# Kernel tuning notes

Measured on AMD Instinct MI355X. Metric: run time of the kernel, lower is better.

## Reference

```python
import jax, jax.numpy as jnp
import numpy as np

BATCH, SEQ_LEN, D_MODEL, STATE = 4, 2048, 64, 64


def setup_inputs() -> dict:
    key = jax.random.key(0)
    ks = jax.random.split(key, 6)
    def w(k, shape):
        return (jax.random.normal(k, shape, jnp.float32) * 0.05)
    return {
        "x": jax.random.normal(ks[0], (BATCH, SEQ_LEN, D_MODEL), jnp.float32),
        "W1": w(ks[1], (D_MODEL, D_MODEL)),  # fc1: d -> d (delta)
        "b1": jnp.zeros((D_MODEL,), jnp.float32),
        "W2": w(ks[2], (D_MODEL, STATE)),    # fc2: d -> n (B)
        "b2": jnp.zeros((STATE,), jnp.float32),
        "W3": w(ks[3], (D_MODEL, STATE)),    # fc3: d -> n (C)
        "b3": jnp.zeros((STATE,), jnp.float32),
        "A": w(ks[4], (D_MODEL, STATE)),     # A parameter [d, n]
    }


def reference(x, W1, b1, W2, b2, W3, b3, A):
    # x: [b, l, d]
    Bm = x @ W2 + b2                               # [b, l, n]
    C = x @ W3 + b3                                # [b, l, n]
    delta = jax.nn.softplus(x @ W1 + b1)           # [b, l, d]
    # discretization (as in original torch code)
    dA = jnp.exp(jnp.einsum('bld,dn->bldn', delta, A))   # [b, l, d, n]
    dB = delta[..., None] * Bm[:, :, None, :]            # [b, l, d, n]
    # h_prev is zeros in the original forward, so dA * h_prev == 0
    h = dA * 0.0 + x[..., None] * dB                     # [b, l, d, n]
    y = jnp.einsum('bln,bldn->bld', C, h)                # [b, l, d]
    return y
```

## Files before the change

### kernel.cpp

```cpp
#include <hip/hip_runtime.h>
#include <cmath>

#define BATCH 4
#define SEQLEN 2048
#define DMODEL 64
#define NTOK (BATCH * SEQLEN)
#define TOK_PER_WAVE 8
#define WAVES_PER_BLOCK 4
#define TOK_PER_BLOCK (TOK_PER_WAVE * WAVES_PER_BLOCK)
#define NBLOCKS (NTOK / TOK_PER_BLOCK)
#define WROW 68

__global__ __launch_bounds__(256, 1) void s6_fused_kernel(
    const float* __restrict__ x,
    const float* __restrict__ W1, const float* __restrict__ b1,
    const float* __restrict__ W2, const float* __restrict__ b2,
    const float* __restrict__ W3, const float* __restrict__ b3,
    float* __restrict__ y)
{
    __shared__ float sWT[3][DMODEL * WROW];

    const int tid = threadIdx.x;

    {
        const float4* gm[3] = { (const float4*)W1, (const float4*)W2, (const float4*)W3 };
        #pragma unroll
        for (int m = 0; m < 3; ++m) {
            #pragma unroll
            for (int i0 = 0; i0 < 4; ++i0) {
                const int i = tid + 256 * i0;
                const float4 w = gm[m][i];
                const int k  = i >> 4;
                const int d0 = (i & 15) << 2;
                sWT[m][(d0 + 0) * WROW + k] = w.x;
                sWT[m][(d0 + 1) * WROW + k] = w.y;
                sWT[m][(d0 + 2) * WROW + k] = w.z;
                sWT[m][(d0 + 3) * WROW + k] = w.w;
            }
        }
    }

    const int lane = tid & 63;
    const int wave = tid >> 6;
    const int tok0 = __builtin_amdgcn_readfirstlane(
        (blockIdx.x * WAVES_PER_BLOCK + wave) * TOK_PER_WAVE);
    const float* __restrict__ xb = x + (size_t)tok0 * DMODEL;

    float xv[TOK_PER_WAVE];
    #pragma unroll
    for (int t = 0; t < TOK_PER_WAVE; ++t)
        xv[t] = x[(size_t)(tok0 + t) * DMODEL + lane];

    float a1[TOK_PER_WAVE], a2[TOK_PER_WAVE], a3[TOK_PER_WAVE];
    const float bb1 = b1[lane], bb2 = b2[lane], bb3 = b3[lane];
    #pragma unroll
    for (int t = 0; t < TOK_PER_WAVE; ++t) { a1[t] = bb1; a2[t] = bb2; a3[t] = bb3; }

    __syncthreads();

    const float* __restrict__ r1 = &sWT[0][lane * WROW];
    const float* __restrict__ r2 = &sWT[1][lane * WROW];
    const float* __restrict__ r3 = &sWT[2][lane * WROW];

    #pragma unroll
    for (int k0 = 0; k0 < DMODEL; k0 += 4) {
        const float4 w1 = *(const float4*)(r1 + k0);
        const float4 w2 = *(const float4*)(r2 + k0);
        const float4 w3 = *(const float4*)(r3 + k0);
        #pragma unroll
        for (int t = 0; t < TOK_PER_WAVE; ++t) {
            const float* xr = xb + t * DMODEL + k0;
            const float x0 = xr[0], x1 = xr[1], x2 = xr[2], x3 = xr[3];
            a1[t] = fmaf(x3, w1.w, fmaf(x2, w1.z, fmaf(x1, w1.y, fmaf(x0, w1.x, a1[t]))));
            a2[t] = fmaf(x3, w2.w, fmaf(x2, w2.z, fmaf(x1, w2.y, fmaf(x0, w2.x, a2[t]))));
            a3[t] = fmaf(x3, w3.w, fmaf(x2, w3.z, fmaf(x1, w3.y, fmaf(x0, w3.x, a3[t]))));
        }
    }

    #pragma unroll
    for (int t = 0; t < TOK_PER_WAVE; ++t) {
        const float delta = log1pf(expf(a1[t]));
        float prod = a2[t] * a3[t];
        #pragma unroll
        for (int off = 32; off > 0; off >>= 1)
            prod += __shfl_xor(prod, off);
        y[(size_t)(tok0 + t) * DMODEL + lane] = xv[t] * delta * prod;
    }
}

extern "C" void kernel_launch(void* const* d_in, const int* in_sizes, int n_in,
                              void* d_out, int out_size, void* d_ws, size_t ws_size,
                              hipStream_t stream) {
    const float* x  = (const float*)d_in[0];
    const float* W1 = (const float*)d_in[1];
    const float* b1 = (const float*)d_in[2];
    const float* W2 = (const float*)d_in[3];
    const float* b2 = (const float*)d_in[4];
    const float* W3 = (const float*)d_in[5];
    const float* b3 = (const float*)d_in[6];
    float* y = (float*)d_out;

    s6_fused_kernel<<<NBLOCKS, 256, 0, stream>>>(x, W1, b1, W2, b2, W3, b3, y);
}
```

Baseline: 14.84 us.

## Halve tokens per wave, XOR-swizzle shared weights, and issue all loads before LDS writes

Cuts tokens per wave from 8 to 4, which doubles the block count, and raises the launch bound to allow two blocks per CU. The padded transposed shared-memory weight layout is replaced by an unpadded layout with an XOR swizzle on float4 slots to avoid bank conflicts. All global weight, x and bias loads are now issued before the LDS stores so their latencies overlap. In exchange, each block reloads and transposes the weights for half as many tokens, which doubles total staging work.

```diff
diff --git a/kernel.cpp b/kernel.cpp
--- a/kernel.cpp
+++ b/kernel.cpp
@@ -5,43 +5,38 @@
 #define SEQLEN 2048
 #define DMODEL 64
 #define NTOK (BATCH * SEQLEN)
-#define TOK_PER_WAVE 8
+#define TOK_PER_WAVE 4
 #define WAVES_PER_BLOCK 4
 #define TOK_PER_BLOCK (TOK_PER_WAVE * WAVES_PER_BLOCK)
 #define NBLOCKS (NTOK / TOK_PER_BLOCK)
-#define WROW 68
 
-__global__ __launch_bounds__(256, 1) void s6_fused_kernel(
+__global__ __launch_bounds__(256, 2) void s6_fused_kernel(
     const float* __restrict__ x,
     const float* __restrict__ W1, const float* __restrict__ b1,
     const float* __restrict__ W2, const float* __restrict__ b2,
     const float* __restrict__ W3, const float* __restrict__ b3,
     float* __restrict__ y)
 {
-    __shared__ float sWT[3][DMODEL * WROW];
+    __shared__ float sW[3][DMODEL * DMODEL];
 
     const int tid = threadIdx.x;
+    const int lane = tid & 63;
+    const int wave = tid >> 6;
 
+    float4 wreg[3][4];
     {
-        const float4* gm[3] = { (const float4*)W1, (const float4*)W2, (const float4*)W3 };
+        const float4* g0 = (const float4*)W1;
+        const float4* g1 = (const float4*)W2;
+        const float4* g2 = (const float4*)W3;
         #pragma unroll
-        for (int m = 0; m < 3; ++m) {
-            #pragma unroll
-            for (int i0 = 0; i0 < 4; ++i0) {
-                const int i = tid + 256 * i0;
-                const float4 w = gm[m][i];
-                const int k  = i >> 4;
-                const int d0 = (i & 15) << 2;
-                sWT[m][(d0 + 0) * WROW + k] = w.x;
-                sWT[m][(d0 + 1) * WROW + k] = w.y;
-                sWT[m][(d0 + 2) * WROW + k] = w.z;
-                sWT[m][(d0 + 3) * WROW + k] = w.w;
-            }
+        for (int i0 = 0; i0 < 4; ++i0) {
+            const int i = tid + 256 * i0;
+            wreg[0][i0] = g0[i];
+            wreg[1][i0] = g1[i];
+            wreg[2][i0] = g2[i];
         }
     }
 
-    const int lane = tid & 63;
-    const int wave = tid >> 6;
     const int tok0 = __builtin_amdgcn_readfirstlane(
         (blockIdx.x * WAVES_PER_BLOCK + wave) * TOK_PER_WAVE);
     const float* __restrict__ xb = x + (size_t)tok0 * DMODEL;
@@ -51,25 +46,44 @@
     for (int t = 0; t < TOK_PER_WAVE; ++t)
         xv[t] = x[(size_t)(tok0 + t) * DMODEL + lane];
 
+    const float bb1 = b1[lane], bb2 = b2[lane], bb3 = b3[lane];
+
+    #pragma unroll
+    for (int m = 0; m < 3; ++m) {
+        #pragma unroll
+        for (int i0 = 0; i0 < 4; ++i0) {
+            const int i  = tid + 256 * i0;
+            const int k  = i >> 4;
+            const int d0 = (i & 15) << 2;
+            const int slot = (((k >> 2) ^ (i & 7)) << 2) + (k & 3);
+            const float* w = (const float*)&wreg[m][i0];
+            float* base = sW[m];
+            #pragma unroll
+            for (int j = 0; j < 4; ++j)
+                base[(d0 + j) * DMODEL + slot] = w[j];
+        }
+    }
+
     float a1[TOK_PER_WAVE], a2[TOK_PER_WAVE], a3[TOK_PER_WAVE];
-    const float bb1 = b1[lane], bb2 = b2[lane], bb3 = b3[lane];
     #pragma unroll
     for (int t = 0; t < TOK_PER_WAVE; ++t) { a1[t] = bb1; a2[t] = bb2; a3[t] = bb3; }
 
     __syncthreads();
 
-    const float* __restrict__ r1 = &sWT[0][lane * WROW];
-    const float* __restrict__ r2 = &sWT[1][lane * WROW];
-    const float* __restrict__ r3 = &sWT[2][lane * WROW];
+    const int swz = (lane >> 2) & 7;
+    const float* __restrict__ r1 = sW[0] + lane * DMODEL;
+    const float* __restrict__ r2 = sW[1] + lane * DMODEL;
+    const float* __restrict__ r3 = sW[2] + lane * DMODEL;
 
     #pragma unroll
-    for (int k0 = 0; k0 < DMODEL; k0 += 4) {
-        const float4 w1 = *(const float4*)(r1 + k0);
-        const float4 w2 = *(const float4*)(r2 + k0);
-        const float4 w3 = *(const float4*)(r3 + k0);
+    for (int kk = 0; kk < DMODEL / 4; ++kk) {
+        const int off = (kk ^ swz) << 2;
+        const float4 w1 = *(const float4*)(r1 + off);
+        const float4 w2 = *(const float4*)(r2 + off);
+        const float4 w3 = *(const float4*)(r3 + off);
         #pragma unroll
         for (int t = 0; t < TOK_PER_WAVE; ++t) {
-            const float* xr = xb + t * DMODEL + k0;
+            const float* xr = xb + t * DMODEL + kk * 4;
             const float x0 = xr[0], x1 = xr[1], x2 = xr[2], x3 = xr[3];
             a1[t] = fmaf(x3, w1.w, fmaf(x2, w1.z, fmaf(x1, w1.y, fmaf(x0, w1.x, a1[t]))));
             a2[t] = fmaf(x3, w2.w, fmaf(x2, w2.z, fmaf(x1, w2.y, fmaf(x0, w2.x, a2[t]))));
```

Result: faster. 13.37 us (-9.9%).
